# Kernel optimization log

Measured on AMD Instinct MI355X. Metric: run time of the kernel, lower is better.

The kernel has to match this reference:

```python
import jax, jax.numpy as jnp
import numpy as np

B, T, C = 4, 2048, 1024
H = 16
HS = C // H          # 64
FF = 4 * C           # 4096
EPS = 1e-5


def layernorm(x, g, b):
    mu = jnp.mean(x, axis=-1, keepdims=True)
    var = jnp.mean(jnp.square(x - mu), axis=-1, keepdims=True)
    return (x - mu) * jax.lax.rsqrt(var + EPS) * g + b


def setup_inputs() -> dict:
    key = jax.random.key(0)
    ks = jax.random.split(key, 16)
    s_in = 1.0 / np.sqrt(C)
    s_ff = 1.0 / np.sqrt(FF)
    return {
        "x": jax.random.normal(ks[0], (B, T, C), jnp.float32),
        # per-head Q/K/V projections stacked: [H, C, HS]
        "Wq": jax.random.normal(ks[1], (H, C, HS), jnp.float32) * s_in,
        "Wk": jax.random.normal(ks[2], (H, C, HS), jnp.float32) * s_in,
        "Wv": jax.random.normal(ks[3], (H, C, HS), jnp.float32) * s_in,
        "Wproj": jax.random.normal(ks[4], (C, C), jnp.float32) * s_in,
        "bproj": jnp.zeros((C,), jnp.float32),
        "W1": jax.random.normal(ks[5], (C, FF), jnp.float32) * s_in,
        "b1": jnp.zeros((FF,), jnp.float32),
        "W2": jax.random.normal(ks[6], (FF, C), jnp.float32) * s_ff,
        "b2": jnp.zeros((C,), jnp.float32),
        "ln1_g": jnp.ones((C,), jnp.float32),
        "ln1_b": jnp.zeros((C,), jnp.float32),
        "ln2_g": jnp.ones((C,), jnp.float32),
        "ln2_b": jnp.zeros((C,), jnp.float32),
    }


def reference(x, Wq, Wk, Wv, Wproj, bproj, W1, b1, W2, b2,
              ln1_g, ln1_b, ln2_g, ln2_b):
    # --- multi-head causal self-attention on layernorm1(x) ---
    h = layernorm(x, ln1_g, ln1_b)                       # [B,T,C]
    q = jnp.einsum('btc,hcd->bhtd', h, Wq)
    k = jnp.einsum('btc,hcd->bhtd', h, Wk)
    v = jnp.einsum('btc,hcd->bhtd', h, Wv)
    scores = jnp.einsum('bhtd,bhsd->bhts', q, k) * (HS ** -0.5)
    causal = jnp.tril(jnp.ones((T, T), bool))
    scores = jnp.where(causal, scores, -jnp.inf)
    att = jax.nn.softmax(scores, axis=-1)                # [B,H,T,T]
    o = jnp.einsum('bhts,bhsd->bthd', att, v).reshape(B, T, C)  # head concat
    x = x + o @ Wproj + bproj
    # --- feedforward on layernorm2(x) ---
    h2 = layernorm(x, ln2_g, ln2_b)
    ff = jax.nn.relu(h2 @ W1 + b1) @ W2 + b2
    return x + ff
```

## Files before the change

### kernel.cpp

```cpp
#include <hip/hip_runtime.h>
#include <cstddef>
#include <cstdio>

#define Bn   4
#define Tn   2048
#define Cn   1024
#define Hn   16
#define HSn  64
#define FFn  4096
#define ROWS (Bn*Tn)
#define QKVW (3*Cn)

typedef __attribute__((ext_vector_type(8))) __bf16 bf16x8;
typedef __attribute__((ext_vector_type(4))) float f32x4;

__device__ __forceinline__ unsigned short f2bf(float f){
  unsigned int u = __float_as_uint(f);
  unsigned int r = (u + 0x7fffu + ((u >> 16) & 1u)) >> 16;
  return (unsigned short)r;
}

#define GLD16(g, l) __builtin_amdgcn_global_load_lds( \
    (__attribute__((address_space(1))) void*)(void*)(g), \
    (__attribute__((address_space(3))) void*)(l), 16, 0, 0)

__device__ __forceinline__ float wave_sum_f(float v){
#pragma unroll
  for (int o = 32; o > 0; o >>= 1) v += __shfl_xor(v, o);
  return v;
}

__global__ void ln_bf16(const float* __restrict__ x, const float* __restrict__ g,
                        const float* __restrict__ bb, unsigned short* __restrict__ y){
  const int row = blockIdx.x;
  const int tid = threadIdx.x;
  const float4 v = reinterpret_cast<const float4*>(x + (size_t)row * Cn)[tid];
  float s  = v.x + v.y + v.z + v.w;
  float ss = v.x*v.x + v.y*v.y + v.z*v.z + v.w*v.w;
  s = wave_sum_f(s); ss = wave_sum_f(ss);
  __shared__ float sm[4], sm2[4];
  const int w = tid >> 6, lane = tid & 63;
  if (lane == 0){ sm[w] = s; sm2[w] = ss; }
  __syncthreads();
  const float tot  = sm[0] + sm[1] + sm[2] + sm[3];
  const float tot2 = sm2[0] + sm2[1] + sm2[2] + sm2[3];
  const float mu = tot * (1.0f / Cn);
  const float rs = rsqrtf(tot2 * (1.0f / Cn) - mu * mu + 1e-5f);
  const float4 gv = reinterpret_cast<const float4*>(g)[tid];
  const float4 bv = reinterpret_cast<const float4*>(bb)[tid];
  ushort4 o;
  o.x = f2bf((v.x - mu) * rs * gv.x + bv.x);
  o.y = f2bf((v.y - mu) * rs * gv.y + bv.y);
  o.z = f2bf((v.z - mu) * rs * gv.z + bv.z);
  o.w = f2bf((v.w - mu) * rs * gv.w + bv.w);
  reinterpret_cast<ushort4*>(y + (size_t)row * Cn)[tid] = o;
}

__global__ void transpose_cast(const float* __restrict__ in, unsigned short* __restrict__ out,
                               int R, int Cc){
  __shared__ float t[64][65];
  const int tid = threadIdx.x;
  const int r0 = blockIdx.y * 64, c0 = blockIdx.x * 64;
  const int rb = tid >> 6, cl = tid & 63;
#pragma unroll
  for (int j = 0; j < 16; ++j)
    t[rb + j*4][cl] = in[(size_t)(r0 + rb + j*4) * Cc + c0 + cl];
  __syncthreads();
#pragma unroll
  for (int j = 0; j < 16; ++j)
    out[(size_t)(c0 + rb + j*4) * R + r0 + cl] = f2bf(t[cl][rb + j*4]);
}

__global__ void repack_qkv_t(const float* __restrict__ Wq, const float* __restrict__ Wk,
                             const float* __restrict__ Wv, unsigned short* __restrict__ Wrt){
  __shared__ float t[64][65];
  const int tid = threadIdx.x;
  const int kb = blockIdx.x * 64;
  const int hh = blockIdx.y;
  const int sec = hh >> 4, h = hh & 15;
  const float* W = (sec == 0) ? Wq : ((sec == 1) ? Wk : Wv);
  const int rb = tid >> 6, dl = tid & 63;
#pragma unroll
  for (int j = 0; j < 16; ++j)
    t[rb + j*4][dl] = W[h * (Cn*HSn) + (size_t)(kb + rb + j*4) * HSn + dl];
  __syncthreads();
#pragma unroll
  for (int j = 0; j < 16; ++j)
    Wrt[(size_t)(sec*Cn + h*64 + rb + j*4) * Cn + kb + dl] = f2bf(t[dl][rb + j*4]);
}

template<int RELU, int OUT_BF16>
__global__ __launch_bounds__(512, 2)
void gemm256(const unsigned short* __restrict__ A, const unsigned short* __restrict__ Bt,
             void* __restrict__ Cout, int M, int N, int K,
             const float* __restrict__ bias, const float* __restrict__ resid){
  __shared__ __align__(16) unsigned short As[4 * 8192];
  __shared__ __align__(16) unsigned short Bs[4 * 8192];
  const int tid  = threadIdx.x;
  const int wid  = tid >> 6, lane = tid & 63;
  const int wm   = wid >> 2, wn = wid & 3;
  const int fr   = lane & 15, Lq = lane >> 4;

  const int id  = blockIdx.x + gridDim.x * blockIdx.y;
  const int Nbn = gridDim.x;
  const int cpx = (gridDim.x * gridDim.y) >> 3;
  const int wg  = (id & 7) * cpx + (id >> 3);
  const int bm  = wg / Nbn;
  const int bn  = wg - bm * Nbn;

  const int srow  = wid * 8 + (lane >> 3);
  const int skoff = (((lane & 7) ^ (srow & 7)) * 8);
  const unsigned short* Abase = A  + (size_t)(bm * 256 + srow) * K + skoff;
  const unsigned short* Bbase = Bt + (size_t)(bn * 256 + srow) * K + skoff;

  auto stA = [&](int t, int h){
    const unsigned short* g0 = Abase + (size_t)h * 128 * K + (size_t)t * 64;
    unsigned short* l0 = As + (((2*t + h) & 3) * 8192) + wid * 512;
    GLD16(g0, l0);
    GLD16(g0 + (size_t)64 * K, l0 + 4096);
  };
  auto stB = [&](int t, int h){
    const unsigned short* g0 = Bbase + (size_t)h * 128 * K + (size_t)t * 64;
    unsigned short* l0 = Bs + (((2*t + h) & 3) * 8192) + wid * 512;
    GLD16(g0, l0);
    GLD16(g0 + (size_t)64 * K, l0 + 4096);
  };

  f32x4 acc[8][4] = {};
  const int NT = K >> 6;

  stA(0, 0); stA(0, 1); stB(0, 0); stB(0, 1);

  for (int t = 0; t < NT; ++t){
    const unsigned short* aS = As + (((2*t + wm) & 3) * 8192);
    const unsigned short* bS = Bs + (((2*t + (wn >> 1)) & 3) * 8192)
                                  + ((wn & 1) * 64) * 64;
    const bool pf = (t + 1 < NT);

    if (pf){ stA(t+1, 0); stA(t+1, 1); stB(t+1, 0); stB(t+1, 1); }
    __builtin_amdgcn_sched_barrier(0);
    if (pf) asm volatile("s_waitcnt vmcnt(8)");
    else    asm volatile("s_waitcnt vmcnt(0)");
    __builtin_amdgcn_s_barrier();

#pragma unroll
    for (int kk = 0; kk < 2; ++kk){
      const int kx = (((kk*4) + Lq) ^ (fr & 7)) * 8;
      bf16x8 bfv[4], af[4];
#pragma unroll
      for (int ni = 0; ni < 4; ++ni)
        bfv[ni] = *reinterpret_cast<const bf16x8*>(&bS[(ni*16 + fr) * 64 + kx]);
#pragma unroll
      for (int m2 = 0; m2 < 4; ++m2)
        af[m2] = *reinterpret_cast<const bf16x8*>(&aS[(m2*16 + fr) * 64 + kx]);
#pragma unroll
      for (int m2 = 0; m2 < 4; ++m2)
#pragma unroll
        for (int ni = 0; ni < 4; ++ni)
          acc[m2][ni] = __builtin_amdgcn_mfma_f32_16x16x32_bf16(
              af[m2], bfv[ni], acc[m2][ni], 0, 0, 0);
#pragma unroll
      for (int m2 = 0; m2 < 4; ++m2)
        af[m2] = *reinterpret_cast<const bf16x8*>(&aS[((4+m2)*16 + fr) * 64 + kx]);
#pragma unroll
      for (int m2 = 0; m2 < 4; ++m2)
#pragma unroll
        for (int ni = 0; ni < 4; ++ni)
          acc[4+m2][ni] = __builtin_amdgcn_mfma_f32_16x16x32_bf16(
              af[m2], bfv[ni], acc[4+m2][ni], 0, 0, 0);
    }
    __builtin_amdgcn_sched_barrier(0);
    __builtin_amdgcn_s_barrier();
  }

  const int lc = fr, lr4 = Lq * 4;
#pragma unroll
  for (int ni = 0; ni < 4; ++ni){
    const int col = bn*256 + wn*64 + ni*16 + lc;
    const float bv = bias ? bias[col] : 0.f;
#pragma unroll
    for (int mi = 0; mi < 8; ++mi){
      const int rowb = bm*256 + wm*128 + mi*16 + lr4;
#pragma unroll
      for (int r = 0; r < 4; ++r){
        float v = acc[mi][ni][r] + bv;
        if (RELU) v = fmaxf(v, 0.f);
        if (resid) v += resid[(size_t)(rowb + r) * N + col];
        if (OUT_BF16)
          ((unsigned short*)Cout)[(size_t)(rowb + r) * N + col] = f2bf(v);
        else
          ((float*)Cout)[(size_t)(rowb + r) * N + col] = v;
      }
    }
  }
}

template<int RELU, int OUT_BF16>
__global__ __launch_bounds__(256, 2)
void gemm128ring(const unsigned short* __restrict__ A, const unsigned short* __restrict__ Bt,
                 void* __restrict__ Cout, int M, int N, int K,
                 const float* __restrict__ bias, const float* __restrict__ resid){
  __shared__ __align__(16) unsigned short As[2 * 8192];
  __shared__ __align__(16) unsigned short Bs[2 * 8192];
  const int tid  = threadIdx.x;
  const int wave = tid >> 6, lane = tid & 63;
  const int wm   = wave >> 1, wn = wave & 1;
  const int fr   = lane & 15, Lq = lane >> 4;

  const int id  = blockIdx.x + gridDim.x * blockIdx.y;
  const int Nbn = gridDim.x;
  const int cpx = (gridDim.x * gridDim.y) >> 3;
  const int wg  = (id & 7) * cpx + (id >> 3);
  const int bm  = wg / Nbn;
  const int bn  = wg - bm * Nbn;

  const int srow  = tid >> 3;
  const int skoff = (((tid & 7) ^ (srow & 7)) * 8);
  const unsigned short* Abase = A  + (size_t)(bm * 128 + srow) * K + skoff;
  const unsigned short* Bbase = Bt + (size_t)(bn * 128 + srow) * K + skoff;

  auto stA = [&](int t){
    const unsigned short* g0 = Abase + (size_t)t * 64;
    unsigned short* l0 = As + ((t & 1) * 8192) + tid * 8;
#pragma unroll
    for (int j = 0; j < 4; ++j)
      GLD16(g0 + (size_t)(j*32) * K, l0 + j*2048);
  };
  auto stB = [&](int t){
    const unsigned short* g0 = Bbase + (size_t)t * 64;
    unsigned short* l0 = Bs + ((t & 1) * 8192) + tid * 8;
#pragma unroll
    for (int j = 0; j < 4; ++j)
      GLD16(g0 + (size_t)(j*32) * K, l0 + j*2048);
  };

  f32x4 acc[4][4] = {};
  const int NT = K >> 6;

  stA(0); stB(0);

  for (int t = 0; t < NT; ++t){
    const unsigned short* aS = As + ((t & 1) * 8192);
    const unsigned short* bS = Bs + ((t & 1) * 8192);
    const bool pf = (t + 1 < NT);

    if (pf){ stA(t+1); stB(t+1); }
    __builtin_amdgcn_sched_barrier(0);
    if (pf) asm volatile("s_waitcnt vmcnt(8)");
    else    asm volatile("s_waitcnt vmcnt(0)");
    __builtin_amdgcn_s_barrier();

#pragma unroll
    for (int kk = 0; kk < 2; ++kk){
      const int kx = (((kk*4) + Lq) ^ (fr & 7)) * 8;
      bf16x8 bfv[4], af[4];
#pragma unroll
      for (int ni = 0; ni < 4; ++ni)
        bfv[ni] = *reinterpret_cast<const bf16x8*>(&bS[(wn*64 + ni*16 + fr) * 64 + kx]);
#pragma unroll
      for (int mi = 0; mi < 4; ++mi)
        af[mi] = *reinterpret_cast<const bf16x8*>(&aS[(wm*64 + mi*16 + fr) * 64 + kx]);
#pragma unroll
      for (int mi = 0; mi < 4; ++mi)
#pragma unroll
        for (int ni = 0; ni < 4; ++ni)
          acc[mi][ni] = __builtin_amdgcn_mfma_f32_16x16x32_bf16(
              af[mi], bfv[ni], acc[mi][ni], 0, 0, 0);
    }
    __builtin_amdgcn_sched_barrier(0);
    __builtin_amdgcn_s_barrier();
  }

  const int lc = fr, lr4 = Lq * 4;
#pragma unroll
  for (int ni = 0; ni < 4; ++ni){
    const int col = bn*128 + wn*64 + ni*16 + lc;
    const float bv = bias ? bias[col] : 0.f;
#pragma unroll
    for (int mi = 0; mi < 4; ++mi){
      const int rowb = bm*128 + wm*64 + mi*16 + lr4;
#pragma unroll
      for (int r = 0; r < 4; ++r){
        float v = acc[mi][ni][r] + bv;
        if (RELU) v = fmaxf(v, 0.f);
        if (resid) v += resid[(size_t)(rowb + r) * N + col];
        if (OUT_BF16)
          ((unsigned short*)Cout)[(size_t)(rowb + r) * N + col] = f2bf(v);
        else
          ((float*)Cout)[(size_t)(rowb + r) * N + col] = v;
      }
    }
  }
}

__global__ void blockify_kv(const unsigned short* __restrict__ qkv,
                            unsigned short* __restrict__ Kb,
                            unsigned short* __restrict__ Vb){
  const int st = blockIdx.x, h = blockIdx.y, b = blockIdx.z;
  const int tid = threadIdx.x;
  const size_t base = ((size_t)(b*Hn + h)*32 + st) * 4096;
#pragma unroll
  for (int it = 0; it < 2; ++it){
    const int idx = it*256 + tid;
    const int s = idx >> 3, d8 = idx & 7;
    const uint4 v = *reinterpret_cast<const uint4*>(
        qkv + (size_t)(b*Tn + st*64 + s)*QKVW + Cn + h*64 + d8*8);
    *reinterpret_cast<uint4*>(Kb + base + d8*512 + ((s ^ d8) * 8)) = v;
  }
#pragma unroll
  for (int it = 0; it < 2; ++it){
    const int idx = it*256 + tid;
    const int d = idx & 63, s8 = idx >> 6;
    unsigned short tmp[8];
#pragma unroll
    for (int j = 0; j < 8; ++j)
      tmp[j] = qkv[(size_t)(b*Tn + st*64 + s8*8 + j)*QKVW + 2*Cn + h*64 + d];
    ushort4 lo, hi;
    lo.x = tmp[0]; lo.y = tmp[1]; lo.z = tmp[2]; lo.w = tmp[3];
    hi.x = tmp[4]; hi.y = tmp[5]; hi.z = tmp[6]; hi.w = tmp[7];
    *reinterpret_cast<ushort4*>(Vb + base + s8*512 + ((d ^ s8) * 8))     = lo;
    *reinterpret_cast<ushort4*>(Vb + base + s8*512 + ((d ^ s8) * 8) + 4) = hi;
  }
}

__global__ __launch_bounds__(256, 2)
void attn_mfma4(const unsigned short* __restrict__ qkv,
                const unsigned short* __restrict__ Kb,
                const unsigned short* __restrict__ Vb,
                unsigned short* __restrict__ O){
  __shared__ __align__(16) unsigned short Pt[4][16][72];

  const int bh = blockIdx.x;
  const int b = bh >> 4, h = bh & 15;
  const int qg = blockIdx.y;
  const int tid = threadIdx.x;
  const int wv = tid >> 6, l = tid & 63;
  const int qblk = (wv == 0) ? qg : (wv == 1) ? (qg + 8)
                 : (wv == 2) ? (23 - qg) : (31 - qg);
  const int Lq = l >> 4, fr = l & 15;

  const size_t kvbase = ((size_t)(b*Hn + h) * 32) * 4096;

  union U { uint4 u; bf16x8 v; };
  U qf[4][2];
  const unsigned short* Qbase = qkv + ((size_t)(b*Tn + qblk*64)) * QKVW + h*64;
#pragma unroll
  for (int f = 0; f < 4; ++f){
    const unsigned short* qr = Qbase + (size_t)(f*16 + fr) * QKVW + Lq*8;
    qf[f][0].u = *reinterpret_cast<const uint4*>(qr);
    qf[f][1].u = *reinterpret_cast<const uint4*>(qr + 32);
  }

  f32x4 Oa[4][4] = {};
  float lsum[4] = {0.f, 0.f, 0.f, 0.f};
  const float C1 = 0.18033688011112042f;
  const float C2 = 28.853900817779268f;

  for (int st = 0; st <= qblk; ++st){
    const unsigned short* Kt = Kb + kvbase + (size_t)st * 4096;
    const unsigned short* Vt = Vb + kvbase + (size_t)st * 4096;

    U k0[4], k1[4];
#pragma unroll
    for (int sb = 0; sb < 4; ++sb){
      const int s = sb*16 + fr;
      k0[sb].u = *reinterpret_cast<const uint4*>(&Kt[ Lq   *512 + ((s ^  Lq   ) * 8)]);
      k1[sb].u = *reinterpret_cast<const uint4*>(&Kt[(4+Lq)*512 + ((s ^ (4+Lq)) * 8)]);
    }
    U v0[4], v1[4];
#pragma unroll
    for (int db = 0; db < 4; ++db){
      const int d = db*16 + fr;
      v0[db].u = *reinterpret_cast<const uint4*>(&Vt[ Lq   *512 + ((d ^  Lq   ) * 8)]);
      v1[db].u = *reinterpret_cast<const uint4*>(&Vt[(4+Lq)*512 + ((d ^ (4+Lq)) * 8)]);
    }

    const bool diag = (st == qblk);
#pragma unroll
    for (int f = 0; f < 4; ++f){
      f32x4 S[4];
#pragma unroll
      for (int sb = 0; sb < 4; ++sb){
        f32x4 z = {0.f, 0.f, 0.f, 0.f};
        z     = __builtin_amdgcn_mfma_f32_16x16x32_bf16(k0[sb].v, qf[f][0].v, z, 0, 0, 0);
        S[sb] = __builtin_amdgcn_mfma_f32_16x16x32_bf16(k1[sb].v, qf[f][1].v, z, 0, 0, 0);
      }
#pragma unroll
      for (int sb = 0; sb < 4; ++sb){
        float p0 = exp2f(fmaf(S[sb][0], C1, -C2));
        float p1 = exp2f(fmaf(S[sb][1], C1, -C2));
        float p2 = exp2f(fmaf(S[sb][2], C1, -C2));
        float p3 = exp2f(fmaf(S[sb][3], C1, -C2));
        if (diag){
          const int s0 = sb*16 + Lq*4, q = f*16 + fr;
          if (s0 + 0 > q) p0 = 0.f;
          if (s0 + 1 > q) p1 = 0.f;
          if (s0 + 2 > q) p2 = 0.f;
          if (s0 + 3 > q) p3 = 0.f;
        }
        lsum[f] += (p0 + p1) + (p2 + p3);
        const unsigned int pk0 = (unsigned int)f2bf(p0) | ((unsigned int)f2bf(p1) << 16);
        const unsigned int pk1 = (unsigned int)f2bf(p2) | ((unsigned int)f2bf(p3) << 16);
        *reinterpret_cast<uint2*>(&Pt[wv][fr][sb*16 + Lq*4]) = make_uint2(pk0, pk1);
      }
      U pf0, pf1;
      pf0.u = *reinterpret_cast<const uint4*>(&Pt[wv][fr][Lq*8]);
      pf1.u = *reinterpret_cast<const uint4*>(&Pt[wv][fr][32 + Lq*8]);
#pragma unroll
      for (int db = 0; db < 4; ++db){
        Oa[db][f] = __builtin_amdgcn_mfma_f32_16x16x32_bf16(v0[db].v, pf0.v, Oa[db][f], 0, 0, 0);
        Oa[db][f] = __builtin_amdgcn_mfma_f32_16x16x32_bf16(v1[db].v, pf1.v, Oa[db][f], 0, 0, 0);
      }
    }
  }

#pragma unroll
  for (int f = 0; f < 4; ++f){
    float s = lsum[f];
    s += __shfl_xor(s, 16);
    s += __shfl_xor(s, 32);
    const float inv = 1.0f / s;
    const size_t orow = (size_t)(b*Tn + qblk*64 + f*16 + fr);
#pragma unroll
    for (int db = 0; db < 4; ++db){
      ushort4 o;
      o.x = f2bf(Oa[db][f][0] * inv);
      o.y = f2bf(Oa[db][f][1] * inv);
      o.z = f2bf(Oa[db][f][2] * inv);
      o.w = f2bf(Oa[db][f][3] * inv);
      *reinterpret_cast<ushort4*>(&O[orow*Cn + h*64 + db*16 + Lq*4]) = o;
    }
  }
}

extern "C" void kernel_launch(void* const* d_in, const int* in_sizes, int n_in,
                              void* d_out, int out_size, void* d_ws, size_t ws_size,
                              hipStream_t stream){
  const float* x     = (const float*)d_in[0];
  const float* Wq    = (const float*)d_in[1];
  const float* Wk    = (const float*)d_in[2];
  const float* Wv    = (const float*)d_in[3];
  const float* Wproj = (const float*)d_in[4];
  const float* bproj = (const float*)d_in[5];
  const float* W1    = (const float*)d_in[6];
  const float* b1    = (const float*)d_in[7];
  const float* W2    = (const float*)d_in[8];
  const float* b2    = (const float*)d_in[9];
  const float* ln1_g = (const float*)d_in[10];
  const float* ln1_b = (const float*)d_in[11];
  const float* ln2_g = (const float*)d_in[12];
  const float* ln2_b = (const float*)d_in[13];
  float* out = (float*)d_out;

  const size_t MB = 1024ull * 1024ull;
  if (ws_size < 192ull * MB){
    fprintf(stderr, "kernel_launch: need 192MB workspace, got %zu\n", ws_size);
    return;
  }
  char* ws = (char*)d_ws;
  float*          x1    = (float*)(ws + 0);
  unsigned short* h     = (unsigned short*)(ws + 32 * MB);
  unsigned short* qkvb  = (unsigned short*)(ws + 48 * MB);
  unsigned short* ff1   = (unsigned short*)(ws + 48 * MB);
  unsigned short* Kb    = (unsigned short*)(ws + 96 * MB);
  unsigned short* Vb    = (unsigned short*)(ws + 112 * MB);
  unsigned short* Ob    = (unsigned short*)(ws + 128 * MB);
  unsigned short* Wrt   = (unsigned short*)(ws + 144 * MB);
  unsigned short* Wpt   = (unsigned short*)(ws + 150 * MB);
  unsigned short* W1t   = (unsigned short*)(ws + 152 * MB);
  unsigned short* W2t   = (unsigned short*)(ws + 160 * MB);

  repack_qkv_t<<<dim3(Cn/64, 3*Hn), 256, 0, stream>>>(Wq, Wk, Wv, Wrt);
  transpose_cast<<<dim3(Cn/64,  Cn/64),  256, 0, stream>>>(Wproj, Wpt, Cn,  Cn);
  transpose_cast<<<dim3(FFn/64, Cn/64),  256, 0, stream>>>(W1,    W1t, Cn,  FFn);
  transpose_cast<<<dim3(Cn/64,  FFn/64), 256, 0, stream>>>(W2,    W2t, FFn, Cn);

  ln_bf16<<<ROWS, 256, 0, stream>>>(x, ln1_g, ln1_b, h);
  gemm256<0,1><<<dim3(QKVW/256, ROWS/256), 512, 0, stream>>>(
      h, Wrt, qkvb, ROWS, QKVW, Cn, nullptr, nullptr);
  blockify_kv<<<dim3(Tn/64, Hn, Bn), 256, 0, stream>>>(qkvb, Kb, Vb);
  attn_mfma4<<<dim3(64, 8), 256, 0, stream>>>(qkvb, Kb, Vb, Ob);
  gemm128ring<0,0><<<dim3(Cn/128, ROWS/128), 256, 0, stream>>>(
      Ob, Wpt, x1, ROWS, Cn, Cn, bproj, x);
  ln_bf16<<<ROWS, 256, 0, stream>>>(x1, ln2_g, ln2_b, h);
  gemm256<1,1><<<dim3(FFn/256, ROWS/256), 512, 0, stream>>>(
      h, W1t, ff1, ROWS, FFn, Cn, b1, nullptr);
  gemm128ring<0,0><<<dim3(Cn/128, ROWS/128), 256, 0, stream>>>(
      ff1, W2t, out, ROWS, Cn, FFn, b2, x1);
}
```

Before: 585.7 us.

## Halve attention query tile per wave to double grid and cut registers

The attention kernel now gives each wave 32 query rows instead of 64 and launches twice as many blocks (64x16). Causal load balancing pairs blocks as qg, qg+16, 47-qg and 63-qg. V tiles are loaded per d-block inside the PV loop rather than all up front, and P is staged per fragment. Together these lower register pressure and add parallelism, at the cost of reading each K/V tile twice as often and doing more diagonal masking work.

```diff
diff --git a/kernel.cpp b/kernel.cpp
--- a/kernel.cpp
+++ b/kernel.cpp
@@ -324,66 +324,62 @@
 }
 
 __global__ __launch_bounds__(256, 2)
-void attn_mfma4(const unsigned short* __restrict__ qkv,
+void attn_mfma5(const unsigned short* __restrict__ qkv,
                 const unsigned short* __restrict__ Kb,
                 const unsigned short* __restrict__ Vb,
                 unsigned short* __restrict__ O){
-  __shared__ __align__(16) unsigned short Pt[4][16][72];
+  __shared__ __align__(16) unsigned short Pt[4][2][16][72];
 
   const int bh = blockIdx.x;
   const int b = bh >> 4, h = bh & 15;
   const int qg = blockIdx.y;
   const int tid = threadIdx.x;
   const int wv = tid >> 6, l = tid & 63;
-  const int qblk = (wv == 0) ? qg : (wv == 1) ? (qg + 8)
-                 : (wv == 2) ? (23 - qg) : (31 - qg);
+  const int qb = (wv == 0) ? qg : (wv == 1) ? (qg + 16)
+               : (wv == 2) ? (47 - qg) : (63 - qg);
   const int Lq = l >> 4, fr = l & 15;
 
   const size_t kvbase = ((size_t)(b*Hn + h) * 32) * 4096;
 
   union U { uint4 u; bf16x8 v; };
-  U qf[4][2];
-  const unsigned short* Qbase = qkv + ((size_t)(b*Tn + qblk*64)) * QKVW + h*64;
-#pragma unroll
-  for (int f = 0; f < 4; ++f){
+  U qf[2][2];
+  const unsigned short* Qbase = qkv + ((size_t)(b*Tn + qb*32)) * QKVW + h*64;
+#pragma unroll
+  for (int f = 0; f < 2; ++f){
     const unsigned short* qr = Qbase + (size_t)(f*16 + fr) * QKVW + Lq*8;
     qf[f][0].u = *reinterpret_cast<const uint4*>(qr);
     qf[f][1].u = *reinterpret_cast<const uint4*>(qr + 32);
   }
 
-  f32x4 Oa[4][4] = {};
-  float lsum[4] = {0.f, 0.f, 0.f, 0.f};
+  f32x4 Oa[4][2] = {};
+  float lsum[2] = {0.f, 0.f};
   const float C1 = 0.18033688011112042f;
   const float C2 = 28.853900817779268f;
 
-  for (int st = 0; st <= qblk; ++st){
+  const int oLo = Lq*512       + ((fr ^ Lq)       * 8);
+  const int oHi = (4+Lq)*512   + ((fr ^ (4+Lq))   * 8);
+
+  const int nst = qb >> 1;
+
+  for (int st = 0; st <= nst; ++st){
     const unsigned short* Kt = Kb + kvbase + (size_t)st * 4096;
     const unsigned short* Vt = Vb + kvbase + (size_t)st * 4096;
-
-    U k0[4], k1[4];
+    const bool diag = (st == nst);
+
+    U klo[4], khi[4];
 #pragma unroll
     for (int sb = 0; sb < 4; ++sb){
-      const int s = sb*16 + fr;
-      k0[sb].u = *reinterpret_cast<const uint4*>(&Kt[ Lq   *512 + ((s ^  Lq   ) * 8)]);
-      k1[sb].u = *reinterpret_cast<const uint4*>(&Kt[(4+Lq)*512 + ((s ^ (4+Lq)) * 8)]);
-    }
-    U v0[4], v1[4];
-#pragma unroll
-    for (int db = 0; db < 4; ++db){
-      const int d = db*16 + fr;
-      v0[db].u = *reinterpret_cast<const uint4*>(&Vt[ Lq   *512 + ((d ^  Lq   ) * 8)]);
-      v1[db].u = *reinterpret_cast<const uint4*>(&Vt[(4+Lq)*512 + ((d ^ (4+Lq)) * 8)]);
-    }
-
-    const bool diag = (st == qblk);
-#pragma unroll
-    for (int f = 0; f < 4; ++f){
+      klo[sb].u = *reinterpret_cast<const uint4*>(Kt + oLo + sb*128);
+      khi[sb].u = *reinterpret_cast<const uint4*>(Kt + oHi + sb*128);
+    }
+#pragma unroll
+    for (int f = 0; f < 2; ++f){
       f32x4 S[4];
 #pragma unroll
       for (int sb = 0; sb < 4; ++sb){
         f32x4 z = {0.f, 0.f, 0.f, 0.f};
-        z     = __builtin_amdgcn_mfma_f32_16x16x32_bf16(k0[sb].v, qf[f][0].v, z, 0, 0, 0);
-        S[sb] = __builtin_amdgcn_mfma_f32_16x16x32_bf16(k1[sb].v, qf[f][1].v, z, 0, 0, 0);
+        z     = __builtin_amdgcn_mfma_f32_16x16x32_bf16(klo[sb].v, qf[f][0].v, z, 0, 0, 0);
+        S[sb] = __builtin_amdgcn_mfma_f32_16x16x32_bf16(khi[sb].v, qf[f][1].v, z, 0, 0, 0);
       }
 #pragma unroll
       for (int sb = 0; sb < 4; ++sb){
@@ -392,7 +388,8 @@
         float p2 = exp2f(fmaf(S[sb][2], C1, -C2));
         float p3 = exp2f(fmaf(S[sb][3], C1, -C2));
         if (diag){
-          const int s0 = sb*16 + Lq*4, q = f*16 + fr;
+          const int s0 = st*64 + sb*16 + Lq*4;
+          const int q  = qb*32 + f*16 + fr;
           if (s0 + 0 > q) p0 = 0.f;
           if (s0 + 1 > q) p1 = 0.f;
           if (s0 + 2 > q) p2 = 0.f;
@@ -401,26 +398,33 @@
         lsum[f] += (p0 + p1) + (p2 + p3);
         const unsigned int pk0 = (unsigned int)f2bf(p0) | ((unsigned int)f2bf(p1) << 16);
         const unsigned int pk1 = (unsigned int)f2bf(p2) | ((unsigned int)f2bf(p3) << 16);
-        *reinterpret_cast<uint2*>(&Pt[wv][fr][sb*16 + Lq*4]) = make_uint2(pk0, pk1);
+        *reinterpret_cast<uint2*>(&Pt[wv][f][fr][sb*16 + Lq*4]) = make_uint2(pk0, pk1);
       }
-      U pf0, pf1;
-      pf0.u = *reinterpret_cast<const uint4*>(&Pt[wv][fr][Lq*8]);
-      pf1.u = *reinterpret_cast<const uint4*>(&Pt[wv][fr][32 + Lq*8]);
-#pragma unroll
-      for (int db = 0; db < 4; ++db){
-        Oa[db][f] = __builtin_amdgcn_mfma_f32_16x16x32_bf16(v0[db].v, pf0.v, Oa[db][f], 0, 0, 0);
-        Oa[db][f] = __builtin_amdgcn_mfma_f32_16x16x32_bf16(v1[db].v, pf1.v, Oa[db][f], 0, 0, 0);
+    }
+
+#pragma unroll
+    for (int db = 0; db < 4; ++db){
+      U vlo, vhi;
+      vlo.u = *reinterpret_cast<const uint4*>(Vt + oLo + db*128);
+      vhi.u = *reinterpret_cast<const uint4*>(Vt + oHi + db*128);
+#pragma unroll
+      for (int f = 0; f < 2; ++f){
+        U pf0, pf1;
+        pf0.u = *reinterpret_cast<const uint4*>(&Pt[wv][f][fr][Lq*8]);
+        pf1.u = *reinterpret_cast<const uint4*>(&Pt[wv][f][fr][32 + Lq*8]);
+        Oa[db][f] = __builtin_amdgcn_mfma_f32_16x16x32_bf16(vlo.v, pf0.v, Oa[db][f], 0, 0, 0);
+        Oa[db][f] = __builtin_amdgcn_mfma_f32_16x16x32_bf16(vhi.v, pf1.v, Oa[db][f], 0, 0, 0);
       }
     }
   }
 
 #pragma unroll
-  for (int f = 0; f < 4; ++f){
+  for (int f = 0; f < 2; ++f){
     float s = lsum[f];
     s += __shfl_xor(s, 16);
     s += __shfl_xor(s, 32);
     const float inv = 1.0f / s;
-    const size_t orow = (size_t)(b*Tn + qblk*64 + f*16 + fr);
+    const size_t orow = (size_t)(b*Tn + qb*32 + f*16 + fr);
 #pragma unroll
     for (int db = 0; db < 4; ++db){
       ushort4 o;
@@ -479,7 +483,7 @@
   gemm256<0,1><<<dim3(QKVW/256, ROWS/256), 512, 0, stream>>>(
       h, Wrt, qkvb, ROWS, QKVW, Cn, nullptr, nullptr);
   blockify_kv<<<dim3(Tn/64, Hn, Bn), 256, 0, stream>>>(qkvb, Kb, Vb);
-  attn_mfma4<<<dim3(64, 8), 256, 0, stream>>>(qkvb, Kb, Vb, Ob);
+  attn_mfma5<<<dim3(64, 16), 256, 0, stream>>>(qkvb, Kb, Vb, Ob);
   gemm128ring<0,0><<<dim3(Cn/128, ROWS/128), 256, 0, stream>>>(
       Ob, Wpt, x1, ROWS, Cn, Cn, bproj, x);
   ln_bf16<<<ROWS, 256, 0, stream>>>(x1, ln2_g, ln2_b, h);
```

Result: faster. 559.2 us (-4.5%).
